# Optimization experiments

Hardware: AMD Instinct MI355X
Metric: run time of the kernel (lower is better)

Reference implementation:

```python
import jax, jax.numpy as jnp
import numpy as np

N_HEADS = 16


def setup_inputs() -> dict:
    key = jax.random.key(0)
    k1, k2, k3 = jax.random.split(key, 3)
    B, T, C = 4, 2048, 1024
    x = jax.random.normal(k1, (B, T, C), dtype=jnp.float32)
    # torch nn.Linear weights are (out_features, in_features); y = x @ W.T
    w_in = jax.random.normal(k2, (3 * C, C), dtype=jnp.float32) * 0.02
    w_out = jax.random.normal(k3, (C, C), dtype=jnp.float32) * 0.02
    return {"x": x, "w_in": w_in, "w_out": w_out}


def reference(x, w_in, w_out):
    B, T, C = x.shape
    H = N_HEADS
    hd = C // H

    qkv = x @ w_in.T                      # [B, T, 3C]
    q, k, v = jnp.split(qkv, 3, axis=2)   # each [B, T, C]

    def heads(t):
        return t.reshape(B, T, H, hd).transpose(0, 2, 1, 3)  # [B, H, T, hd]

    q, k, v = heads(q), heads(k), heads(v)

    scale = 1.0 / jnp.sqrt(jnp.float32(hd))
    scores = jnp.einsum('bhqd,bhkd->bhqk', q, k) * scale      # [B, H, T, T]
    causal = jnp.tril(jnp.ones((T, T), dtype=bool))
    scores = jnp.where(causal, scores, -jnp.inf)
    attn = jax.nn.softmax(scores, axis=-1)
    y = jnp.einsum('bhqk,bhkd->bhqd', attn, v)                # [B, H, T, hd]
    y = y.transpose(0, 2, 1, 3).reshape(B, T, C)
    return y @ w_out.T
```

## Files before the change

kernel.cpp:

```cpp
#include <hip/hip_runtime.h>
#include <stdint.h>

#define BB 4
#define TT 2048
#define CC 1024
#define HH 16
#define HD 64
#define C3 3072
#define MM (BB*TT)

typedef __bf16 bf16_t;
typedef bf16_t bf16x8 __attribute__((ext_vector_type(8)));
typedef float f32x4 __attribute__((ext_vector_type(4)));
typedef unsigned short u16;
typedef u16 u16x8 __attribute__((ext_vector_type(8)));
typedef uint32_t u32;

static __device__ __forceinline__ u16 f2bf(float f){
  u32 u = __builtin_bit_cast(u32, f);
  u32 r = (u + 0x7fffu + ((u >> 16) & 1u)) >> 16;
  return (u16)r;
}

static __device__ __forceinline__ f32x4 mfma16(bf16x8 a, bf16x8 b, f32x4 c){
  return __builtin_amdgcn_mfma_f32_16x16x32_bf16(a, b, c, 0, 0, 0);
}

typedef __attribute__((address_space(1))) void* gas_t;
typedef __attribute__((address_space(3))) void* las_t;
static __device__ __forceinline__ void gload16(const void* g, void* l){
  __builtin_amdgcn_global_load_lds((gas_t)g, (las_t)l, 16, 0, 0);
}

__global__ __launch_bounds__(256) void cvt_all(const float* __restrict__ x,
                                               const float* __restrict__ wi,
                                               const float* __restrict__ wo,
                                               u16* __restrict__ out){
  const int n1 = MM*CC/8, n2 = C3*CC/8, n3 = CC*CC/8;
  const int total = n1 + n2 + n3;
  int stride = gridDim.x * blockDim.x;
  for (int i = blockIdx.x * blockDim.x + threadIdx.x; i < total; i += stride){
    const float* src; int k;
    if (i < n1){ src = x; k = i; }
    else if (i < n1 + n2){ src = wi; k = i - n1; }
    else { src = wo; k = i - n1 - n2; }
    const float4* p = (const float4*)src + (size_t)k * 2;
    float4 a = p[0], b = p[1];
    u16x8 o;
    o[0]=f2bf(a.x); o[1]=f2bf(a.y); o[2]=f2bf(a.z); o[3]=f2bf(a.w);
    o[4]=f2bf(b.x); o[5]=f2bf(b.y); o[6]=f2bf(b.z); o[7]=f2bf(b.w);
    *((u16x8*)out + i) = o;
  }
}

template<int OUTBF>
__global__ __launch_bounds__(256) void gemm_bt(const u16* __restrict__ A,
                                               const u16* __restrict__ Bm,
                                               void* __restrict__ Cp,
                                               int M, int N, int K,
                                               int nbx, int cpx){
  __shared__ u16 As[128*64];
  __shared__ u16 Bs[128*64];
  const int bid = blockIdx.x;
  const int nb = (bid & 7) * cpx + (bid >> 3);
  const int by = nb / nbx, bx = nb - by * nbx;
  const int tid  = threadIdx.x;
  const int lane = tid & 63;
  const int w    = tid >> 6;
  const int m0   = by * 128;
  const int n0   = bx * 128;
  const int wm   = (w >> 1) * 64;
  const int wn   = (w & 1) * 64;
  const int lr   = lane & 15;
  const int lg4  = lane >> 4;

  f32x4 acc[4][4] = {};

  const int rq  = tid >> 3;
  const int c8s = ((tid & 7) ^ (rq & 7)) * 8;
  const u16* gA = A  + (size_t)(m0 + rq) * K + c8s;
  const u16* gB = Bm + (size_t)(n0 + rq) * K + c8s;
  char* lA = (char*)As + tid*16;
  char* lB = (char*)Bs + tid*16;

  for (int k0 = 0; k0 < K; k0 += 64){
    #pragma unroll
    for (int q = 0; q < 4; q++){
      gload16(gA + (size_t)(q*32)*K + k0, lA + q*4096);
      gload16(gB + (size_t)(q*32)*K + k0, lB + q*4096);
    }
    __syncthreads();
    #pragma unroll
    for (int kk = 0; kk < 2; kk++){
      bf16x8 af[4], bfr[4];
      #pragma unroll
      for (int m = 0; m < 4; m++){
        int row = wm + m*16 + lr;
        int slot = ((kk<<2) | lg4) ^ (row & 7);
        af[m] = *(const bf16x8*)((const char*)As + row*128 + slot*16);
      }
      #pragma unroll
      for (int n = 0; n < 4; n++){
        int row = wn + n*16 + lr;
        int slot = ((kk<<2) | lg4) ^ (row & 7);
        bfr[n] = *(const bf16x8*)((const char*)Bs + row*128 + slot*16);
      }
      #pragma unroll
      for (int m = 0; m < 4; m++)
        #pragma unroll
        for (int n = 0; n < 4; n++)
          acc[m][n] = mfma16(af[m], bfr[n], acc[m][n]);
    }
    __syncthreads();
  }

  const int cr = lg4 * 4;
  #pragma unroll
  for (int m = 0; m < 4; m++)
    #pragma unroll
    for (int n = 0; n < 4; n++)
      #pragma unroll
      for (int j = 0; j < 4; j++){
        size_t row = (size_t)(m0 + wm + m*16 + cr + j);
        size_t col = (size_t)(n0 + wn + n*16 + lr);
        if (OUTBF) ((u16*)Cp)[row*(size_t)N + col] = f2bf(acc[m][n][j]);
        else       ((float*)Cp)[row*(size_t)N + col] = acc[m][n][j];
      }
}

__global__ __launch_bounds__(256, 2) void attn_fwd(const u16* __restrict__ qkv,
                                                   u16* __restrict__ y){
  __shared__ u16 Kl[2][64*72];
  __shared__ u16 Vt[2][64*72];
  const int bid = blockIdx.x;
  const int tq = bid >> 6;
  const int h = bid & 15, b = (bid >> 4) & 3;
  const int tid = threadIdx.x, lane = tid & 63, w = tid >> 6;
  const int lr = lane & 15, lg = lane >> 4;
  const size_t base = (size_t)b * TT * C3;
  const int qA = tq*64 + w*16;
  const int qB = (31-tq)*64 + w*16;
  const float SC = 0.18033688011112042f;

  bf16x8 qf[2][2];
  {
    const u16* qp0 = qkv + base + (size_t)(qA + lr) * C3 + h*HD;
    qf[0][0] = *(const bf16x8*)(qp0 + lg*8);
    qf[0][1] = *(const bf16x8*)(qp0 + 32 + lg*8);
    const u16* qp1 = qkv + base + (size_t)(qB + lr) * C3 + h*HD;
    qf[1][0] = *(const bf16x8*)(qp1 + lg*8);
    qf[1][1] = *(const bf16x8*)(qp1 + 32 + lg*8);
    #pragma unroll
    for (int m = 0; m < 2; m++)
      #pragma unroll
      for (int i = 0; i < 2; i++)
        #pragma unroll
        for (int e = 0; e < 8; e++)
          qf[m][i][e] = (bf16_t)((float)qf[m][i][e] * SC);
  }

  const int rK = tid >> 3, cK = tid & 7;
  const int rp = tid & 15;
  const int dc = (tid >> 4) & 7;
  const int hf = tid >> 7;
  const u16* gK = qkv + base + (size_t)rK * C3 + CC + h*HD + cK*8;
  const u16* gV = qkv + base + (size_t)(2*rp + 32*hf) * C3 + 2*CC + h*HD + dc*8;

  const int kkey = ((rK >> 3) & 1) << 5;
  const int kw0 = rK*72 + ((cK*8) ^ kkey);
  const int kw1 = (rK+32)*72 + ((cK*8) ^ kkey);
  const int vcol = ((2*rp + 32*hf) ^ (8*dc)) ^ (32*(dc & 1));

  const int rdx = ((lr >> 2) & 1) << 5;
  const int rbase = 8*(lr >> 2) + (lr & 3);

  u16x8 kreg[2], vreg[2];
  kreg[0] = *(const u16x8*)(gK);
  kreg[1] = *(const u16x8*)(gK + (size_t)32*C3);
  vreg[0] = *(const u16x8*)(gV);
  vreg[1] = *(const u16x8*)(gV + C3);

  f32x4 o[2][4] = {};
  float mj[2] = {-1e30f, -1e30f};
  float lj[2] = {0.f, 0.f};

  const int ktmax = 31 - tq;
  for (int kt = 0; kt <= ktmax; kt++){
    const int cb = kt & 1;
    u16* KL = Kl[cb];
    u16* VT = Vt[cb];
    *(u16x8*)&KL[kw0] = kreg[0];
    *(u16x8*)&KL[kw1] = kreg[1];
    #pragma unroll
    for (int e = 0; e < 8; e++){
      u32 pk = (u32)vreg[0][e] | ((u32)vreg[1][e] << 16);
      *(u32*)&VT[(dc*8+e)*72 + vcol] = pk;
    }
    __syncthreads();

    if (kt < ktmax){
      const u16* gk2 = gK + (size_t)(kt+1)*64*C3;
      const u16* gv2 = gV + (size_t)(kt+1)*64*C3;
      kreg[0] = *(const u16x8*)(gk2);
      kreg[1] = *(const u16x8*)(gk2 + (size_t)32*C3);
      vreg[0] = *(const u16x8*)(gv2);
      vreg[1] = *(const u16x8*)(gv2 + C3);
    }

    const bool m0act = (kt <= tq);
    bf16x8 vb[8];

    #pragma unroll
    for (int m = 1; m >= 0; m--){
      if (m == 0 && !m0act) continue;

      f32x4 s[4] = {};
      __builtin_amdgcn_s_setprio(1);
      #pragma unroll
      for (int n = 0; n < 4; n++){
        const int rho = 32*(n>>1) + 4*(n&1) + rbase;
        bf16x8 kb0 = *(const bf16x8*)&KL[rho*72 + ((     lg*8) ^ rdx)];
        bf16x8 kb1 = *(const bf16x8*)&KL[rho*72 + ((32 + lg*8) ^ rdx)];
        s[n] = mfma16(kb0, qf[m][0], s[n]);
        s[n] = mfma16(kb1, qf[m][1], s[n]);
      }
      __builtin_amdgcn_s_setprio(0);

      if (m == 1){
        #pragma unroll
        for (int n = 0; n < 4; n++){
          const int dcr = (2*n + (lr >> 3)) & 7;
          const int c0 = ((lg ^ dcr) ^ (4 * (dcr & 1))) * 8;
          vb[2*n]   = *(const bf16x8*)&VT[(n*16+lr)*72 + c0];
          vb[2*n+1] = *(const bf16x8*)&VT[(n*16+lr)*72 + (c0 ^ 32)];
        }
      }

      const int qrow = (m ? qB : qA) + lr;
      const bool dm = (kt == (m ? ktmax : tq));
      if (dm){
        #pragma unroll
        for (int n = 0; n < 4; n++)
          #pragma unroll
          for (int j = 0; j < 4; j++)
            if (kt*64 + 32*(n>>1) + 8*lg + 4*(n&1) + j > qrow)
              s[n][j] = -1e30f;
      }
      float x0 = fmaxf(fmaxf(s[0][0], s[0][1]), fmaxf(s[0][2], s[0][3]));
      float x1 = fmaxf(fmaxf(s[1][0], s[1][1]), fmaxf(s[1][2], s[1][3]));
      float x2 = fmaxf(fmaxf(s[2][0], s[2][1]), fmaxf(s[2][2], s[2][3]));
      float x3 = fmaxf(fmaxf(s[3][0], s[3][1]), fmaxf(s[3][2], s[3][3]));
      float tm = fmaxf(fmaxf(x0, x1), fmaxf(x2, x3));
      tm = fmaxf(tm, __shfl_xor(tm, 16, 64));
      tm = fmaxf(tm, __shfl_xor(tm, 32, 64));
      float mo = mj[m];
      if (!__all(tm <= mo + 4.0f)){
        float mn = fmaxf(mo, tm);
        float al = __builtin_amdgcn_exp2f(mo - mn);
        mj[m] = mn;
        lj[m] *= al;
        float a0 = __shfl(al, lg*4+0, 16);
        float a1 = __shfl(al, lg*4+1, 16);
        float a2 = __shfl(al, lg*4+2, 16);
        float a3 = __shfl(al, lg*4+3, 16);
        #pragma unroll
        for (int n = 0; n < 4; n++){
          o[m][n][0] *= a0; o[m][n][1] *= a1;
          o[m][n][2] *= a2; o[m][n][3] *= a3;
        }
      }
      float mm = mj[m];
      float psn[4];
      bf16x8 pa, pb;
      #pragma unroll
      for (int n = 0; n < 4; n++){
        float p0 = __builtin_amdgcn_exp2f(s[n][0] - mm);
        float p1 = __builtin_amdgcn_exp2f(s[n][1] - mm);
        float p2 = __builtin_amdgcn_exp2f(s[n][2] - mm);
        float p3 = __builtin_amdgcn_exp2f(s[n][3] - mm);
        psn[n] = (p0 + p1) + (p2 + p3);
        if (n == 0){ pa[0]=(bf16_t)p0; pa[1]=(bf16_t)p1; pa[2]=(bf16_t)p2; pa[3]=(bf16_t)p3; }
        if (n == 1){ pa[4]=(bf16_t)p0; pa[5]=(bf16_t)p1; pa[6]=(bf16_t)p2; pa[7]=(bf16_t)p3; }
        if (n == 2){ pb[0]=(bf16_t)p0; pb[1]=(bf16_t)p1; pb[2]=(bf16_t)p2; pb[3]=(bf16_t)p3; }
        if (n == 3){ pb[4]=(bf16_t)p0; pb[5]=(bf16_t)p1; pb[6]=(bf16_t)p2; pb[7]=(bf16_t)p3; }
      }
      float ps = (psn[0] + psn[1]) + (psn[2] + psn[3]);
      ps += __shfl_xor(ps, 16, 64);
      ps += __shfl_xor(ps, 32, 64);
      lj[m] += ps;

      __builtin_amdgcn_s_setprio(1);
      #pragma unroll
      for (int n = 0; n < 4; n++){
        o[m][n] = mfma16(pa, vb[2*n],   o[m][n]);
        o[m][n] = mfma16(pb, vb[2*n+1], o[m][n]);
      }
      __builtin_amdgcn_s_setprio(0);
    }
  }

  #pragma unroll
  for (int m = 0; m < 2; m++){
    float inv = 1.0f / lj[m];
    float i0 = __shfl(inv, lg*4+0, 16);
    float i1 = __shfl(inv, lg*4+1, 16);
    float i2 = __shfl(inv, lg*4+2, 16);
    float i3 = __shfl(inv, lg*4+3, 16);
    const int qb = (m ? qB : qA);
    #pragma unroll
    for (int j = 0; j < 4; j++){
      float ij = (j==0) ? i0 : (j==1) ? i1 : (j==2) ? i2 : i3;
      size_t row = (size_t)b*TT + qb + lg*4 + j;
      #pragma unroll
      for (int n = 0; n < 4; n++)
        y[row*CC + h*HD + n*16 + lr] = f2bf(o[m][n][j] * ij);
    }
  }
}

extern "C" void kernel_launch(void* const* d_in, const int* in_sizes, int n_in,
                              void* d_out, int out_size, void* d_ws, size_t ws_size,
                              hipStream_t stream){
  const float* x     = (const float*)d_in[0];
  const float* w_in  = (const float*)d_in[1];
  const float* w_out = (const float*)d_in[2];
  float* out = (float*)d_out;

  u16* xb   = (u16*)d_ws;
  u16* wib  = xb  + (size_t)MM * CC;
  u16* wob  = wib + (size_t)C3 * CC;
  u16* qkvb = wob + (size_t)CC * CC;
  u16* yb   = xb;

  cvt_all<<<2048, 256, 0, stream>>>(x, w_in, w_out, xb);

  gemm_bt<1><<<1536, 256, 0, stream>>>(xb, wib, (void*)qkvb, MM, C3, CC, 24, 192);
  attn_fwd<<<1024, 256, 0, stream>>>(qkvb, yb);
  gemm_bt<0><<<512, 256, 0, stream>>>(yb, wob, (void*)out, MM, CC, CC, 8, 64);
}
```

Baseline: 164.8 us.

## Double-buffer GEMM LDS tiles to overlap global loads with MFMA

Converts the bf16 GEMM main loop to a two-stage LDS ping-pong, issuing the next K-tile's direct-to-LDS loads before computing on the current tile. This lets global-memory latency hide behind MFMA work instead of stalling at a barrier each iteration. It also raises wave priority around the MFMA block. LDS use doubles to 64KB per block, which may reduce occupancy, and the barrier and waitcnt placement needs care to stay race-free.

```diff
diff --git a/kernel.cpp b/kernel.cpp
--- a/kernel.cpp
+++ b/kernel.cpp
@@ -59,8 +59,8 @@
                                                void* __restrict__ Cp,
                                                int M, int N, int K,
                                                int nbx, int cpx){
-  __shared__ u16 As[128*64];
-  __shared__ u16 Bs[128*64];
+  __shared__ u16 As[2][128*64];
+  __shared__ u16 Bs[2][128*64];
   const int bid = blockIdx.x;
   const int nb = (bid & 7) * cpx + (bid >> 3);
   const int by = nb / nbx, bx = nb - by * nbx;
@@ -80,16 +80,26 @@
   const int c8s = ((tid & 7) ^ (rq & 7)) * 8;
   const u16* gA = A  + (size_t)(m0 + rq) * K + c8s;
   const u16* gB = Bm + (size_t)(n0 + rq) * K + c8s;
-  char* lA = (char*)As + tid*16;
-  char* lB = (char*)Bs + tid*16;
-
-  for (int k0 = 0; k0 < K; k0 += 64){
+
+  auto stage = [&](int buf, int t){
+    char* lA = (char*)&As[buf][0] + tid*16;
+    char* lB = (char*)&Bs[buf][0] + tid*16;
     #pragma unroll
     for (int q = 0; q < 4; q++){
-      gload16(gA + (size_t)(q*32)*K + k0, lA + q*4096);
-      gload16(gB + (size_t)(q*32)*K + k0, lB + q*4096);
-    }
-    __syncthreads();
+      gload16(gA + (size_t)(q*32)*K + t*64, lA + q*4096);
+      gload16(gB + (size_t)(q*32)*K + t*64, lB + q*4096);
+    }
+  };
+
+  stage(0, 0);
+
+  const int NT = K >> 6;
+  for (int t = 0; t < NT; t++){
+    const int c = t & 1;
+    asm volatile("s_waitcnt vmcnt(0)" ::: "memory");
+    __builtin_amdgcn_s_barrier();
+    __builtin_amdgcn_sched_barrier(0);
+    if (t + 1 < NT) stage(c ^ 1, t + 1);
     #pragma unroll
     for (int kk = 0; kk < 2; kk++){
       bf16x8 af[4], bfr[4];
@@ -97,21 +107,23 @@
       for (int m = 0; m < 4; m++){
         int row = wm + m*16 + lr;
         int slot = ((kk<<2) | lg4) ^ (row & 7);
-        af[m] = *(const bf16x8*)((const char*)As + row*128 + slot*16);
+        af[m] = *(const bf16x8*)((const char*)&As[c][0] + row*128 + slot*16);
       }
       #pragma unroll
       for (int n = 0; n < 4; n++){
         int row = wn + n*16 + lr;
         int slot = ((kk<<2) | lg4) ^ (row & 7);
-        bfr[n] = *(const bf16x8*)((const char*)Bs + row*128 + slot*16);
-      }
+        bfr[n] = *(const bf16x8*)((const char*)&Bs[c][0] + row*128 + slot*16);
+      }
+      __builtin_amdgcn_s_setprio(1);
       #pragma unroll
       for (int m = 0; m < 4; m++)
         #pragma unroll
         for (int n = 0; n < 4; n++)
           acc[m][n] = mfma16(af[m], bfr[n], acc[m][n]);
-    }
-    __syncthreads();
+      __builtin_amdgcn_s_setprio(0);
+    }
+    __builtin_amdgcn_s_barrier();
   }
 
   const int cr = lg4 * 4;
```

Result: no change. 161.9 us (-1.8%).
